# Optimization experiments

Hardware: AMD Instinct MI355X
Metric: run time of the kernel (lower is better)

## Reference

```python
import jax, jax.numpy as jnp
import numpy as np

LATENT, CTX, HID, TDIM, HEADS = 512, 512, 1024, 128, 8
HEAD_DIM = HID // HEADS
SCALE = HEAD_DIM ** -0.5


def _ln(x, g, b, eps=1e-5):
    m = jnp.mean(x, axis=-1, keepdims=True)
    v = jnp.mean((x - m) ** 2, axis=-1, keepdims=True)
    return (x - m) * jax.lax.rsqrt(v + eps) * g + b


def _time_embed(t):
    half = TDIM // 2
    exponent = jnp.linspace(0.0, 1.0, half, dtype=t.dtype)
    freqs = jnp.exp(jnp.log(1000.0) * exponent)
    ang = 2.0 * jnp.pi * t[:, None] * freqs[None, :]
    return jnp.concatenate([jnp.sin(ang), jnp.cos(ang)], axis=-1)  # [B, TDIM]


def setup_inputs() -> dict:
    key = jax.random.key(0)
    ks = iter(jax.random.split(key, 32))
    B, M = 4096, 64

    def w(k, i, o):
        return jax.random.normal(k, (i, o), jnp.float32) * 0.02

    inp = {
        "states": jax.random.normal(next(ks), (B, LATENT), jnp.float32),
        "time_values": jax.random.uniform(next(ks), (B,), jnp.float32),
        "class_summary": jax.random.normal(next(ks), (B, CTX), jnp.float32),
        "support_memory": jax.random.normal(next(ks), (B, M, LATENT), jnp.float32),
        # state_trunk: LN(latent+tdim) -> Linear -> GELU -> Linear
        "trunk_ln_g": jnp.ones((LATENT + TDIM,)), "trunk_ln_b": jnp.zeros((LATENT + TDIM,)),
        "trunk_w1": w(next(ks), LATENT + TDIM, HID), "trunk_b1": jnp.zeros((HID,)),
        "trunk_w2": w(next(ks), HID, HID), "trunk_b2": jnp.zeros((HID,)),
        # memory adapter: LN(latent) -> Linear(latent, hid)
        "mem_ln_g": jnp.ones((LATENT,)), "mem_ln_b": jnp.zeros((LATENT,)),
        "mem_w": w(next(ks), LATENT, HID), "mem_b": jnp.zeros((HID,)),
        # attention projections
        "wq": w(next(ks), HID, HID), "bq": jnp.zeros((HID,)),
        "wk": w(next(ks), HID, HID), "bk": jnp.zeros((HID,)),
        "wv": w(next(ks), HID, HID), "bv": jnp.zeros((HID,)),
        "wo": w(next(ks), HID, HID), "bo": jnp.zeros((HID,)),
        # pre-condition norm + FiLM
        "pre_ln_g": jnp.ones((HID,)), "pre_ln_b": jnp.zeros((HID,)),
        "film_w": w(next(ks), CTX, 2 * HID), "film_b": jnp.zeros((2 * HID,)),
        # conditioner: LN -> Linear -> GELU -> Linear
        "cond_ln_g": jnp.ones((HID,)), "cond_ln_b": jnp.zeros((HID,)),
        "cond_w1": w(next(ks), HID, HID), "cond_b1": jnp.zeros((HID,)),
        "cond_w2": w(next(ks), HID, HID), "cond_b2": jnp.zeros((HID,)),
        # output head: LN -> Linear -> GELU -> Linear(hid, latent)
        "head_ln_g": jnp.ones((HID,)), "head_ln_b": jnp.zeros((HID,)),
        "head_w1": w(next(ks), HID, HID), "head_b1": jnp.zeros((HID,)),
        "head_w2": w(next(ks), HID, LATENT), "head_b2": jnp.zeros((LATENT,)),
    }
    return inp


def _forward(states, time_values, class_summary, support_memory,
             trunk_ln_g, trunk_ln_b, trunk_w1, trunk_b1, trunk_w2, trunk_b2,
             mem_ln_g, mem_ln_b, mem_w, mem_b,
             wq, bq, wk, bk, wv, bv, wo, bo,
             pre_ln_g, pre_ln_b, film_w, film_b,
             cond_ln_g, cond_ln_b, cond_w1, cond_b1, cond_w2, cond_b2,
             head_ln_g, head_ln_b, head_w1, head_b1, head_w2, head_b2):
    B, M, _ = support_memory.shape
    gelu = lambda x: jax.nn.gelu(x, approximate=False)

    # trunk: g = Trunk([y, gamma(t)])
    te = _time_embed(time_values)
    x = _ln(jnp.concatenate([states, te], axis=-1), trunk_ln_g, trunk_ln_b)
    g = gelu(x @ trunk_w1 + trunk_b1) @ trunk_w2 + trunk_b2  # [B, HID]

    # encode memory + single-query multi-head attention
    mem_h = _ln(support_memory, mem_ln_g, mem_ln_b) @ mem_w + mem_b  # [B, M, HID]
    q = (g @ wq + bq).reshape(B, HEADS, HEAD_DIM)
    k = (mem_h @ wk + bk).reshape(B, M, HEADS, HEAD_DIM)
    v = (mem_h @ wv + bv).reshape(B, M, HEADS, HEAD_DIM)
    logits = jnp.einsum("bhd,bmhd->bhm", q, k) * SCALE
    attn = jax.nn.softmax(logits, axis=-1)
    summary = jnp.einsum("bhm,bmhd->bhd", attn, v).reshape(B, HID)
    attn_summary = summary @ wo + bo

    # FiLM conditioning
    combined = _ln(g + attn_summary, pre_ln_g, pre_ln_b)
    film = class_summary @ film_w + film_b
    scale, shift = film[:, :HID], film[:, HID:]
    combined = (1.0 + scale) * combined + shift
    cond_x = _ln(combined, cond_ln_g, cond_ln_b)
    conditioned = gelu(cond_x @ cond_w1 + cond_b1) @ cond_w2 + cond_b2 + combined

    # output head
    hx = _ln(conditioned, head_ln_g, head_ln_b)
    return gelu(hx @ head_w1 + head_b1) @ head_w2 + head_b2  # [B, LATENT]


def reference(states, time_values, class_summary, support_memory,
              trunk_ln_g, trunk_ln_b, trunk_w1, trunk_b1, trunk_w2, trunk_b2,
              mem_ln_g, mem_ln_b, mem_w, mem_b,
              wq, bq, wk, bk, wv, bv, wo, bo,
              pre_ln_g, pre_ln_b, film_w, film_b,
              cond_ln_g, cond_ln_b, cond_w1, cond_b1, cond_w2, cond_b2,
              head_ln_g, head_ln_b, head_w1, head_b1, head_w2, head_b2):
    return _forward(states, time_values, class_summary, support_memory,
                    trunk_ln_g, trunk_ln_b, trunk_w1, trunk_b1, trunk_w2, trunk_b2,
                    mem_ln_g, mem_ln_b, mem_w, mem_b,
                    wq, bq, wk, bk, wv, bv, wo, bo,
                    pre_ln_g, pre_ln_b, film_w, film_b,
                    cond_ln_g, cond_ln_b, cond_w1, cond_b1, cond_w2, cond_b2,
                    head_ln_g, head_ln_b, head_w1, head_b1, head_w2, head_b2)
```

## Files before the change

### kernel.cpp

```cpp
#include <hip/hip_runtime.h>
#include <cstdint>
#include <cstddef>

typedef unsigned short ushort_t;
typedef short s16x8 __attribute__((ext_vector_type(8)));
typedef float f32x4 __attribute__((ext_vector_type(4)));

__device__ __forceinline__ float bf2f(ushort_t h){
  union { unsigned int u; float f; } v; v.u = ((unsigned int)h) << 16; return v.f;
}
__device__ __forceinline__ ushort_t f2bf(float x){
  union { float f; unsigned int u; } v; v.f = x;
  unsigned int r = v.u + 0x7FFFu + ((v.u >> 16) & 1u);
  return (ushort_t)(r >> 16);
}
__device__ __forceinline__ float gelu_f(float x){
  return 0.5f * x * (1.0f + erff(x * 0.7071067811865475f));
}
__device__ __forceinline__ float wave_sum(float v){
  #pragma unroll
  for (int o = 32; o; o >>= 1) v += __shfl_xor(v, o);
  return v;
}
__device__ __forceinline__ void block_reduce2(float& s, float& q, float* red){
  s = wave_sum(s); q = wave_sum(q);
  int w = threadIdx.x >> 6, lane = threadIdx.x & 63, nw = blockDim.x >> 6;
  if (lane == 0){ red[w] = s; red[8 + w] = q; }
  __syncthreads();
  float ts = 0.f, tq = 0.f;
  for (int i = 0; i < nw; ++i){ ts += red[i]; tq += red[8 + i]; }
  __syncthreads();
  s = ts; q = tq;
}

#define SSLOT(cc, m) (((cc) & 56) | (((cc) & 7) ^ (((m) ^ ((m) >> 3)) & 7)))

struct TDesc { const float* in; ushort_t* out; int K; int N; int start; };
struct PrepArgs {
  const float* states; const float* tv; const float* lng; const float* lnb; ushort_t* xnb;
  TDesc t[11];
  int ntiles_end;
  int cast1_blocks;
  int cast_end;
  const float* memw; ushort_t* memwb;
  const float* csum; ushort_t* csb;
  const float* memb; const float* wv; const float* bvp; float* bv2;
};

__global__ __launch_bounds__(256) void prep_k(PrepArgs a){
  int bid = blockIdx.x, tid = threadIdx.x;
  __shared__ float buf[640];
  __shared__ float red[16];
  __shared__ float tbuf[32][33];
  if (bid < 4096){
    int row = bid;
    float t = a.tv[row];
    for (int i = tid; i < 640; i += 256){
      float v;
      if (i < 512) v = a.states[(size_t)row * 512 + i];
      else {
        int j = i - 512, jj = j & 63;
        float fr = expf(6.907755278982137f * ((float)jj * (1.0f / 63.0f)));
        float ang = 6.283185307179586f * t * fr;
        v = (j < 64) ? sinf(ang) : cosf(ang);
      }
      buf[i] = v;
    }
    __syncthreads();
    float s = 0.f, q = 0.f;
    for (int i = tid; i < 640; i += 256){ float v = buf[i]; s += v; q += v * v; }
    block_reduce2(s, q, red);
    float mean = s * (1.0f / 640.0f);
    float var = q * (1.0f / 640.0f) - mean * mean;
    float rstd = rsqrtf(var + 1e-5f);
    for (int i = tid; i < 640; i += 256)
      a.xnb[(size_t)row * 640 + i] = f2bf((buf[i] - mean) * rstd * a.lng[i] + a.lnb[i]);
    return;
  }
  bid -= 4096;
  if (bid < a.ntiles_end){
    int d = 0;
    #pragma unroll
    for (int i = 1; i < 11; ++i) if (bid >= a.t[i].start) d = i;
    TDesc td = a.t[d];
    int tile = bid - td.start;
    int tilesx = td.N >> 5;
    int n0 = (tile % tilesx) << 5, k0 = (tile / tilesx) << 5;
    int tx = tid & 31, ty = tid >> 5;
    #pragma unroll
    for (int j = 0; j < 32; j += 8)
      tbuf[ty + j][tx] = td.in[(size_t)(k0 + ty + j) * td.N + (n0 + tx)];
    __syncthreads();
    #pragma unroll
    for (int j = 0; j < 32; j += 8)
      td.out[(size_t)(n0 + ty + j) * td.K + (k0 + tx)] = f2bf(tbuf[tx][ty + j]);
  } else if (bid < a.cast_end){
    int ci = bid - a.ntiles_end;
    const float* src; ushort_t* dst; int i;
    if (ci < a.cast1_blocks){ src = a.memw; dst = a.memwb; i = ci * 1024 + tid * 4; }
    else { src = a.csum; dst = a.csb; i = (ci - a.cast1_blocks) * 1024 + tid * 4; }
    float4 v = *(const float4*)(src + i);
    union { ushort_t u[4]; uint2 p; } pk;
    pk.u[0] = f2bf(v.x); pk.u[1] = f2bf(v.y); pk.u[2] = f2bf(v.z); pk.u[3] = f2bf(v.w);
    *(uint2*)(dst + i) = pk.p;
  } else {
    int col = (bid - a.cast_end) * 256 + tid;
    float a0 = 0.f, a1 = 0.f, a2 = 0.f, a3 = 0.f;
    for (int j = 0; j < 1024; j += 4){
      a0 += a.memb[j + 0] * a.wv[(size_t)(j + 0) * 1024 + col];
      a1 += a.memb[j + 1] * a.wv[(size_t)(j + 1) * 1024 + col];
      a2 += a.memb[j + 2] * a.wv[(size_t)(j + 2) * 1024 + col];
      a3 += a.memb[j + 3] * a.wv[(size_t)(j + 3) * 1024 + col];
    }
    a.bv2[col] = a0 + a1 + a2 + a3 + a.bvp[col];
  }
}

__global__ __launch_bounds__(256) void ln_rows_k(const ushort_t* __restrict__ in, const float* __restrict__ g,
    const float* __restrict__ b, ushort_t* __restrict__ out, int D){
  int row = blockIdx.x, tid = threadIdx.x, i = tid * 4;
  __shared__ float red[16];
  union { uint2 p; ushort_t u[4]; } vv;
  vv.p = *(const uint2*)(in + (size_t)row * D + i);
  float v[4] = { bf2f(vv.u[0]), bf2f(vv.u[1]), bf2f(vv.u[2]), bf2f(vv.u[3]) };
  float s = v[0] + v[1] + v[2] + v[3];
  float q = v[0]*v[0] + v[1]*v[1] + v[2]*v[2] + v[3]*v[3];
  block_reduce2(s, q, red);
  float invD = 1.0f / (float)D;
  float mean = s * invD, var = q * invD - mean * mean, rstd = rsqrtf(var + 1e-5f);
  union { ushort_t u[4]; uint2 p; } pk;
  #pragma unroll
  for (int e = 0; e < 4; ++e) pk.u[e] = f2bf((v[e] - mean) * rstd * g[i + e] + b[i + e]);
  *(uint2*)(out + (size_t)row * D + i) = pk.p;
}

__global__ __launch_bounds__(256) void fuse_film_k(const ushort_t* __restrict__ combb, const ushort_t* __restrict__ filmb,
    const float* __restrict__ pg, const float* __restrict__ pb,
    const float* __restrict__ cg, const float* __restrict__ cb,
    ushort_t* __restrict__ c2b, ushort_t* __restrict__ cxb){
  int row = blockIdx.x, tid = threadIdx.x, i = tid * 4;
  __shared__ float red[16];
  union { uint2 p; ushort_t u[4]; } av;
  av.p = *(const uint2*)(combb + (size_t)row * 1024 + i);
  float x[4] = { bf2f(av.u[0]), bf2f(av.u[1]), bf2f(av.u[2]), bf2f(av.u[3]) };
  float s = x[0] + x[1] + x[2] + x[3];
  float q = x[0]*x[0] + x[1]*x[1] + x[2]*x[2] + x[3]*x[3];
  block_reduce2(s, q, red);
  float mean = s * (1.0f / 1024.0f), var = q * (1.0f / 1024.0f) - mean * mean;
  float rstd = rsqrtf(var + 1e-5f);
  float4 pgv = *(const float4*)(pg + i), pbv = *(const float4*)(pb + i);
  union { uint2 p; ushort_t u[4]; } scv, shv;
  scv.p = *(const uint2*)(filmb + (size_t)row * 2048 + i);
  shv.p = *(const uint2*)(filmb + (size_t)row * 2048 + 1024 + i);
  float c2[4];
  {
    float pgx[4] = { pgv.x, pgv.y, pgv.z, pgv.w };
    float pbx[4] = { pbv.x, pbv.y, pbv.z, pbv.w };
    #pragma unroll
    for (int e = 0; e < 4; ++e){
      float cc = (x[e] - mean) * rstd * pgx[e] + pbx[e];
      c2[e] = (1.0f + bf2f(scv.u[e])) * cc + bf2f(shv.u[e]);
    }
  }
  union { ushort_t u[4]; uint2 p; } pc;
  #pragma unroll
  for (int e = 0; e < 4; ++e) pc.u[e] = f2bf(c2[e]);
  *(uint2*)(c2b + (size_t)row * 1024 + i) = pc.p;
  float s2 = c2[0] + c2[1] + c2[2] + c2[3];
  float q2 = c2[0]*c2[0] + c2[1]*c2[1] + c2[2]*c2[2] + c2[3]*c2[3];
  block_reduce2(s2, q2, red);
  float m2 = s2 * (1.0f / 1024.0f), v2 = q2 * (1.0f / 1024.0f) - m2 * m2;
  float r2 = rsqrtf(v2 + 1e-5f);
  float4 cgv = *(const float4*)(cg + i), cbv = *(const float4*)(cb + i);
  union { ushort_t u[4]; uint2 p; } pk;
  pk.u[0] = f2bf((c2[0] - m2) * r2 * cgv.x + cbv.x);
  pk.u[1] = f2bf((c2[1] - m2) * r2 * cgv.y + cbv.y);
  pk.u[2] = f2bf((c2[2] - m2) * r2 * cgv.z + cbv.z);
  pk.u[3] = f2bf((c2[3] - m2) * r2 * cgv.w + cbv.w);
  *(uint2*)(cxb + (size_t)row * 1024 + i) = pk.p;
}

__global__ __launch_bounds__(256, 2) void suppattn_k(
    const float* __restrict__ support, const float* __restrict__ lgw, const float* __restrict__ lbw,
    const ushort_t* __restrict__ U, ushort_t* __restrict__ R)
{
  __shared__ ushort_t S[64 * 512];
  __shared__ ushort_t UG[9 * 512];
  __shared__ float WTf[8][65];
  __shared__ float SUMV[64], SUMSQ[64];
  __shared__ __align__(16) float MEANR[64];
  __shared__ __align__(16) float RSTDR[64];
  __shared__ float PMAX[4][8], PSUM[4][8], PMU[4][8];
  __shared__ float AB[2][8];
  __shared__ float MUH[8];

  int bb = blockIdx.x, tid = threadIdx.x, w = tid >> 6, l = tid & 63;
  const ushort_t* Ub = U + (size_t)bb * 4096;

  for (int id = tid; id < 576; id += 256){
    int hr8 = id >> 6, cc = id & 63;
    int byteoff = hr8 * 1024 + (((cc & 56) | ((cc & 7) ^ (hr8 & 7))) << 4);
    uint4* dst = (uint4*)((char*)UG + byteoff);
    if (hr8 < 8){
      s16x8 uv = *(const s16x8*)(Ub + hr8 * 512 + cc * 8);
      float4 g0 = *(const float4*)(lgw + cc * 8);
      float4 g1 = *(const float4*)(lgw + cc * 8 + 4);
      float ga[8] = { g0.x, g0.y, g0.z, g0.w, g1.x, g1.y, g1.z, g1.w };
      union { ushort_t u[8]; uint4 p; } pk;
      #pragma unroll
      for (int e = 0; e < 8; ++e) pk.u[e] = f2bf(ga[e] * bf2f((ushort_t)uv[e]));
      *dst = pk.p;
    } else {
      *dst = make_uint4(0x3F803F80u, 0x3F803F80u, 0x3F803F80u, 0x3F803F80u);
    }
  }

  {
    int h0 = 2 * w, h1 = 2 * w + 1;
    s16x8 u0 = *(const s16x8*)(Ub + h0 * 512 + l * 8);
    s16x8 u1 = *(const s16x8*)(Ub + h1 * 512 + l * 8);
    float4 g0 = *(const float4*)(lgw + l * 8), g1 = *(const float4*)(lgw + l * 8 + 4);
    float4 c0 = *(const float4*)(lbw + l * 8), c1 = *(const float4*)(lbw + l * 8 + 4);
    float ga[8] = { g0.x, g0.y, g0.z, g0.w, g1.x, g1.y, g1.z, g1.w };
    float ba[8] = { c0.x, c0.y, c0.z, c0.w, c1.x, c1.y, c1.z, c1.w };
    float A0 = 0.f, B0 = 0.f, A1 = 0.f, B1 = 0.f;
    #pragma unroll
    for (int e = 0; e < 8; ++e){
      float x0 = bf2f((ushort_t)u0[e]), x1 = bf2f((ushort_t)u1[e]);
      A0 += ba[e] * x0; B0 += ga[e] * x0;
      A1 += ba[e] * x1; B1 += ga[e] * x1;
    }
    A0 = wave_sum(A0); B0 = wave_sum(B0); A1 = wave_sum(A1); B1 = wave_sum(B1);
    if (l == 0){ AB[0][h0] = A0; AB[1][h0] = B0; AB[0][h1] = A1; AB[1][h1] = B1; }
  }

  #pragma unroll 4
  for (int i = 0; i < 16; ++i){
    int m = i * 4 + w;
    const float* row = support + ((size_t)bb * 64 + m) * 512 + l * 8;
    float4 a0 = *(const float4*)row, a1 = *(const float4*)(row + 4);
    union { ushort_t u[8]; uint4 p; } pk;
    pk.u[0] = f2bf(a0.x); pk.u[1] = f2bf(a0.y); pk.u[2] = f2bf(a0.z); pk.u[3] = f2bf(a0.w);
    pk.u[4] = f2bf(a1.x); pk.u[5] = f2bf(a1.y); pk.u[6] = f2bf(a1.z); pk.u[7] = f2bf(a1.w);
    int byteoff = m * 1024 + (SSLOT(l, m) << 4);
    *(uint4*)((char*)S + byteoff) = pk.p;
  }
  __syncthreads();

  int l15 = l & 15, lk = l >> 4;
  int hr = (l15 < 8) ? l15 : 8;
  int arowb = (w * 16 + l15) * 1024;
  int hrowb = hr * 1024;
  int am = w * 16 + l15;
  f32x4 dacc = (f32x4){0.f, 0.f, 0.f, 0.f};
  f32x4 sacc = (f32x4){0.f, 0.f, 0.f, 0.f};
  #pragma unroll
  for (int ks = 0; ks < 16; ++ks){
    int cc = ks * 4 + lk;
    s16x8 afr = *(const s16x8*)((char*)S + arowb + (SSLOT(cc, am) << 4));
    s16x8 bfr = *(const s16x8*)((char*)UG + hrowb + (((cc & 56) | ((cc & 7) ^ (hr & 7))) << 4));
    dacc = __builtin_amdgcn_mfma_f32_16x16x32_bf16(afr, bfr, dacc, 0, 0, 0);
    sacc = __builtin_amdgcn_mfma_f32_16x16x32_bf16(afr, afr, sacc, 0, 0, 0);
  }
  if (l15 == 8){
    #pragma unroll
    for (int j = 0; j < 4; ++j) SUMV[w * 16 + lk * 4 + j] = dacc[j];
  }
  if ((l15 >> 2) == lk) SUMSQ[w * 16 + l15] = sacc[l15 & 3];
  __syncthreads();
  if (tid < 64){
    float mean = SUMV[tid] * (1.0f / 512.0f);
    float var = SUMSQ[tid] * (1.0f / 512.0f) - mean * mean;
    MEANR[tid] = mean;
    RSTDR[tid] = rsqrtf(var + 1e-5f);
  }
  __syncthreads();

  int r0 = w * 16 + lk * 4;
  float4 mns = *(const float4*)(MEANR + r0);
  float4 rst = *(const float4*)(RSTDR + r0);
  float mn[4] = { mns.x, mns.y, mns.z, mns.w };
  float rs[4] = { rst.x, rst.y, rst.z, rst.w };
  float Ah = AB[0][l15 & 7], Bh = AB[1][l15 & 7];
  float lg[4];
  #pragma unroll
  for (int j = 0; j < 4; ++j)
    lg[j] = 0.08838834764831845f * (rs[j] * (dacc[j] - mn[j] * Bh) + Ah);
  float lmax = fmaxf(fmaxf(lg[0], lg[1]), fmaxf(lg[2], lg[3]));
  lmax = fmaxf(lmax, __shfl_xor(lmax, 16));
  lmax = fmaxf(lmax, __shfl_xor(lmax, 32));
  if (l < 8) PMAX[w][l] = lmax;
  __syncthreads();
  float gmax = fmaxf(fmaxf(PMAX[0][l15 & 7], PMAX[1][l15 & 7]),
                     fmaxf(PMAX[2][l15 & 7], PMAX[3][l15 & 7]));
  float e4[4]; float ls = 0.f, lm = 0.f;
  #pragma unroll
  for (int j = 0; j < 4; ++j){
    e4[j] = __expf(lg[j] - gmax);
    ls += e4[j];
    lm += e4[j] * rs[j] * mn[j];
  }
  ls += __shfl_xor(ls, 16); ls += __shfl_xor(ls, 32);
  lm += __shfl_xor(lm, 16); lm += __shfl_xor(lm, 32);
  if (l < 8){ PSUM[w][l] = ls; PMU[w][l] = lm; }
  __syncthreads();
  float Sh = PSUM[0][l15 & 7] + PSUM[1][l15 & 7] + PSUM[2][l15 & 7] + PSUM[3][l15 & 7];
  float inv = 1.0f / Sh;
  if (l15 < 8){
    #pragma unroll
    for (int j = 0; j < 4; ++j) WTf[l15][r0 + j] = e4[j] * rs[j] * inv;
  }
  if (w == 0 && l < 8){
    MUH[l] = (PMU[0][l] + PMU[1][l] + PMU[2][l] + PMU[3][l]) * inv;
  }
  __syncthreads();

  union { ushort_t u[8]; s16x8 v; } af0, af1;
  af0.v = (s16x8){0,0,0,0,0,0,0,0};
  af1.v = (s16x8){0,0,0,0,0,0,0,0};
  if (l15 < 8){
    #pragma unroll
    for (int e = 0; e < 8; ++e){
      af0.u[e] = f2bf(WTf[l15][lk * 8 + e]);
      af1.u[e] = f2bf(WTf[l15][32 + lk * 8 + e]);
    }
  }
  float mu[4];
  #pragma unroll
  for (int j = 0; j < 4; ++j) mu[j] = (lk < 2) ? MUH[lk * 4 + j] : 0.f;

  const char* Sp = (const char*)S;
  #pragma unroll
  for (int ns = 0; ns < 8; ++ns){
    int c = w * 128 + ns * 16 + l15;
    int cch = c >> 3, cb = (c & 7) * 2;
    int sb = cch & 56, cl = cch & 7;
    union { ushort_t u[8]; s16x8 v; } bf0, bf1;
    #pragma unroll
    for (int e = 0; e < 8; ++e){
      int m0 = lk * 8 + e;
      int m1 = m0 + 32;
      bf0.u[e] = *(const ushort_t*)(Sp + m0 * 1024 + ((sb | (cl ^ ((m0 ^ lk) & 7))) << 4) + cb);
      bf1.u[e] = *(const ushort_t*)(Sp + m1 * 1024 + ((sb | (cl ^ ((m1 ^ (4 + lk)) & 7))) << 4) + cb);
    }
    f32x4 cacc = (f32x4){0.f, 0.f, 0.f, 0.f};
    cacc = __builtin_amdgcn_mfma_f32_16x16x32_bf16(af0.v, bf0.v, cacc, 0, 0, 0);
    cacc = __builtin_amdgcn_mfma_f32_16x16x32_bf16(af1.v, bf1.v, cacc, 0, 0, 0);
    if (lk < 2){
      float gc = lgw[c], bc = lbw[c];
      #pragma unroll
      for (int j = 0; j < 4; ++j){
        int h = lk * 4 + j;
        R[(size_t)bb * 4096 + h * 512 + c] = f2bf(gc * (cacc[j] - mu[j]) + bc);
      }
    }
  }
}

#define GLL16(gsrc, ldst) \
  __builtin_amdgcn_global_load_lds((const __attribute__((address_space(1))) unsigned int*)(gsrc), \
                                   (__attribute__((address_space(3))) unsigned int*)(ldst), 16, 0, 0)

template<bool GELU, bool BIAS, bool WF32, bool WBF16, bool RESID>
__global__ __launch_bounds__(256, 3) void gemm_k(
    const ushort_t* __restrict__ A, int lda, long long aZ,
    const ushort_t* __restrict__ Bt, int ldb, long long bZ,
    const float* __restrict__ bias, long long biasZ,
    float* __restrict__ C, int ldc, long long cZ,
    ushort_t* __restrict__ Cb, int ldcb, long long cbZ,
    const ushort_t* __restrict__ R, int ldr,
    int M, int N, int K)
{
  __shared__ ushort_t smA[2][64 * 64];
  __shared__ ushort_t smB[2][128 * 64];
  int tid = threadIdx.x, lane = tid & 63, w = tid >> 6;
  int z = blockIdx.z;
  A  += (size_t)aZ * z;
  Bt += (size_t)bZ * z;
  if (BIAS)  bias += (size_t)biasZ * z;
  if (WF32)  C    += (size_t)cZ * z;
  if (WBF16) Cb   += (size_t)cbZ * z;

  int gx = gridDim.x, gy = gridDim.y;
  int nwg = gx * gy;
  int bx = blockIdx.x, by = blockIdx.y;
  if ((nwg & 7) == 0 && (gx & (gx - 1)) == 0){
    int lid = bx + gx * by;
    int cpx = nwg >> 3;
    int slid = (lid & 7) * cpx + (lid >> 3);
    int lgx = 31 - __clz(gx);
    bx = slid & (gx - 1);
    by = slid >> lgx;
  }
  int m0 = by * 64, n0 = bx * 128;
  int nk = K >> 6;

  auto stage = [&](int buf, int kt){
    int k0 = kt << 6;
    #pragma unroll
    for (int i = 0; i < 2; ++i){
      int c = ((w << 1) + i) * 64 + lane;
      int rowl = c >> 3, sp = c & 7;
      int sg = sp ^ (rowl & 7);
      GLL16(A + (size_t)(m0 + rowl) * lda + (k0 + sg * 8), &smA[buf][((w << 1) + i) * 512]);
    }
    #pragma unroll
    for (int i = 0; i < 4; ++i){
      int c = ((w << 2) + i) * 64 + lane;
      int rowl = c >> 3, sp = c & 7;
      int sg = sp ^ (rowl & 7);
      GLL16(Bt + (size_t)(n0 + rowl) * ldb + (k0 + sg * 8), &smB[buf][((w << 2) + i) * 512]);
    }
  };

  int qrow = w >> 1, qcol = w & 1;
  int l15 = lane & 15, lk = lane >> 4, l7 = lane & 7;
  int sb0 = ((0 + lk) ^ l7) << 4;
  int sb1 = ((4 + lk) ^ l7) << 4;
  int arow = (qrow * 32 + l15) * 128;
  int brow = (qcol * 64 + l15) * 128;

  f32x4 acc[2][4];
  #pragma unroll
  for (int m = 0; m < 2; ++m)
    #pragma unroll
    for (int n = 0; n < 4; ++n)
      acc[m][n] = (f32x4){0.f, 0.f, 0.f, 0.f};

  stage(0, 0);
  asm volatile("s_waitcnt vmcnt(0)" ::: "memory");
  __syncthreads();
  for (int kt = 0; kt < nk; ++kt){
    int cur = kt & 1;
    if (kt + 1 < nk) stage((kt + 1) & 1, kt + 1);
    const char* ab = (const char*)&smA[cur][0];
    const char* bbp = (const char*)&smB[cur][0];
    s16x8 af[2][2], bfv[4][2];
    #pragma unroll
    for (int m = 0; m < 2; ++m){
      af[m][0] = *(const s16x8*)(ab + arow + m * 2048 + sb0);
      af[m][1] = *(const s16x8*)(ab + arow + m * 2048 + sb1);
    }
    #pragma unroll
    for (int n = 0; n < 4; ++n){
      bfv[n][0] = *(const s16x8*)(bbp + brow + n * 2048 + sb0);
      bfv[n][1] = *(const s16x8*)(bbp + brow + n * 2048 + sb1);
    }
    #pragma unroll
    for (int kb = 0; kb < 2; ++kb)
      #pragma unroll
      for (int m = 0; m < 2; ++m)
        #pragma unroll
        for (int n = 0; n < 4; ++n)
          acc[m][n] = __builtin_amdgcn_mfma_f32_16x16x32_bf16(af[m][kb], bfv[n][kb], acc[m][n], 0, 0, 0);
    asm volatile("s_waitcnt vmcnt(0)" ::: "memory");
    __syncthreads();
  }

  #pragma unroll
  for (int n = 0; n < 4; ++n){
    int col = n0 + qcol * 64 + n * 16 + l15;
    float bvv = BIAS ? bias[col] : 0.0f;
    #pragma unroll
    for (int m = 0; m < 2; ++m){
      int rbase = m0 + qrow * 32 + m * 16 + lk * 4;
      #pragma unroll
      for (int r = 0; r < 4; ++r){
        float x = acc[m][n][r] + bvv;
        if (GELU) x = gelu_f(x);
        int row = rbase + r;
        if (RESID) x += bf2f(R[(size_t)row * ldr + col]);
        if (WF32)  C[(size_t)row * ldc + col] = x;
        if (WBF16) Cb[(size_t)row * ldcb + col] = f2bf(x);
      }
    }
  }
}

extern "C" void kernel_launch(void* const* d_in, const int* in_sizes, int n_in,
                              void* d_out, int out_size, void* d_ws, size_t ws_size,
                              hipStream_t stream)
{
  (void)in_sizes; (void)n_in; (void)out_size;
  const float* states      = (const float*)d_in[0];
  const float* time_values = (const float*)d_in[1];
  const float* class_sum   = (const float*)d_in[2];
  const float* support     = (const float*)d_in[3];
  const float* trunk_ln_g  = (const float*)d_in[4];
  const float* trunk_ln_b  = (const float*)d_in[5];
  const float* trunk_w1    = (const float*)d_in[6];
  const float* trunk_b1    = (const float*)d_in[7];
  const float* trunk_w2    = (const float*)d_in[8];
  const float* trunk_b2    = (const float*)d_in[9];
  const float* mem_ln_g    = (const float*)d_in[10];
  const float* mem_ln_b    = (const float*)d_in[11];
  const float* mem_w       = (const float*)d_in[12];
  const float* mem_b       = (const float*)d_in[13];
  const float* wq          = (const float*)d_in[14];
  const float* bq          = (const float*)d_in[15];
  const float* wk          = (const float*)d_in[16];
  const float* wv          = (const float*)d_in[18];
  const float* bvp         = (const float*)d_in[19];
  const float* wo          = (const float*)d_in[20];
  const float* bo          = (const float*)d_in[21];
  const float* pre_g       = (const float*)d_in[22];
  const float* pre_b       = (const float*)d_in[23];
  const float* film_w      = (const float*)d_in[24];
  const float* film_b      = (const float*)d_in[25];
  const float* cond_g      = (const float*)d_in[26];
  const float* cond_b      = (const float*)d_in[27];
  const float* cond_w1     = (const float*)d_in[28];
  const float* cond_b1     = (const float*)d_in[29];
  const float* cond_w2     = (const float*)d_in[30];
  const float* cond_b2     = (const float*)d_in[31];
  const float* head_g      = (const float*)d_in[32];
  const float* head_bb     = (const float*)d_in[33];
  const float* head_w1     = (const float*)d_in[34];
  const float* head_b1     = (const float*)d_in[35];
  const float* head_w2     = (const float*)d_in[36];
  const float* head_b2     = (const float*)d_in[37];
  float* out = (float*)d_out;

  char* ws = (char*)d_ws;
  size_t off = 0;
  auto alloc = [&](size_t bytes)->char*{
    char* p = ws + off;
    off += (bytes + 255) & ~(size_t)255;
    return p;
  };
  ushort_t* tw1T   = (ushort_t*)alloc((size_t)640 * 1024 * 2);
  ushort_t* tw2T   = (ushort_t*)alloc((size_t)1024 * 1024 * 2);
  ushort_t* wqT    = (ushort_t*)alloc((size_t)1024 * 1024 * 2);
  ushort_t* wkT    = (ushort_t*)alloc((size_t)1024 * 1024 * 2);
  ushort_t* wvT    = (ushort_t*)alloc((size_t)1024 * 1024 * 2);
  ushort_t* woT    = (ushort_t*)alloc((size_t)1024 * 1024 * 2);
  ushort_t* memw_b = (ushort_t*)alloc((size_t)512 * 1024 * 2);
  ushort_t* filmWT = (ushort_t*)alloc((size_t)512 * 2048 * 2);
  ushort_t* cw1T   = (ushort_t*)alloc((size_t)1024 * 1024 * 2);
  ushort_t* cw2T   = (ushort_t*)alloc((size_t)1024 * 1024 * 2);
  ushort_t* hw1T   = (ushort_t*)alloc((size_t)1024 * 1024 * 2);
  ushort_t* hw2T   = (ushort_t*)alloc((size_t)1024 * 512 * 2);
  ushort_t* K2     = (ushort_t*)alloc((size_t)512 * 1024 * 2);
  ushort_t* V2T    = (ushort_t*)alloc((size_t)1024 * 512 * 2);
  float*    bv2    = (float*)   alloc((size_t)1024 * 4);
  ushort_t* xnb    = (ushort_t*)alloc((size_t)4096 * 640 * 2);
  ushort_t* h1     = (ushort_t*)alloc((size_t)4096 * 1024 * 2);
  ushort_t* gb     = (ushort_t*)alloc((size_t)4096 * 1024 * 2);
  ushort_t* qb     = (ushort_t*)alloc((size_t)4096 * 1024 * 2);
  ushort_t* U      = (ushort_t*)alloc((size_t)4096 * 4096 * 2);
  ushort_t* Rb     = (ushort_t*)alloc((size_t)4096 * 4096 * 2);
  ushort_t* sumb   = (ushort_t*)alloc((size_t)4096 * 1024 * 2);
  ushort_t* combb  = (ushort_t*)alloc((size_t)4096 * 1024 * 2);
  ushort_t* csb    = (ushort_t*)alloc((size_t)4096 * 512 * 2);
  ushort_t* filmb  = (ushort_t*)alloc((size_t)4096 * 2048 * 2);
  ushort_t* c2b    = (ushort_t*)alloc((size_t)4096 * 1024 * 2);
  ushort_t* cxb    = (ushort_t*)alloc((size_t)4096 * 1024 * 2);
  ushort_t* c1     = (ushort_t*)alloc((size_t)4096 * 1024 * 2);
  ushort_t* cond2b = (ushort_t*)alloc((size_t)4096 * 1024 * 2);
  ushort_t* hxb    = (ushort_t*)alloc((size_t)4096 * 1024 * 2);
  ushort_t* h3     = (ushort_t*)alloc((size_t)4096 * 1024 * 2);
  if (off > ws_size) return;

  PrepArgs pa;
  pa.states = states; pa.tv = time_values; pa.lng = trunk_ln_g; pa.lnb = trunk_ln_b; pa.xnb = xnb;
  int s = 0;
  auto setT = [&](int i, const float* in, ushort_t* o, int K, int N){
    pa.t[i].in = in; pa.t[i].out = o; pa.t[i].K = K; pa.t[i].N = N; pa.t[i].start = s;
    s += (N >> 5) * (K >> 5);
  };
  setT(0, trunk_w1, tw1T, 640, 1024);
  setT(1, trunk_w2, tw2T, 1024, 1024);
  setT(2, wq, wqT, 1024, 1024);
  setT(3, wk, wkT, 1024, 1024);
  setT(4, wv, wvT, 1024, 1024);
  setT(5, wo, woT, 1024, 1024);
  setT(6, film_w, filmWT, 512, 2048);
  setT(7, cond_w1, cw1T, 1024, 1024);
  setT(8, cond_w2, cw2T, 1024, 1024);
  setT(9, head_w1, hw1T, 1024, 1024);
  setT(10, head_w2, hw2T, 1024, 512);
  pa.ntiles_end = s;
  pa.cast1_blocks = (512 * 1024) / 1024;
  pa.cast_end = s + pa.cast1_blocks + (4096 * 512) / 1024;
  pa.memw = mem_w; pa.memwb = memw_b;
  pa.csum = class_sum; pa.csb = csb;
  pa.memb = mem_b; pa.wv = wv; pa.bvp = bvp; pa.bv2 = bv2;
  prep_k<<<4096 + pa.cast_end + 4, 256, 0, stream>>>(pa);

  gemm_k<false, false, false, true, false><<<dim3(8, 8, 1), 256, 0, stream>>>(
      memw_b, 1024, 0, wkT, 1024, 0, nullptr, 0, nullptr, 0, 0, K2, 1024, 0, nullptr, 0, 512, 1024, 1024);
  gemm_k<false, false, false, true, false><<<dim3(4, 16, 1), 256, 0, stream>>>(
      wvT, 1024, 0, memw_b, 1024, 0, nullptr, 0, nullptr, 0, 0, V2T, 512, 0, nullptr, 0, 1024, 512, 1024);

  gemm_k<true, true, false, true, false><<<dim3(8, 64, 1), 256, 0, stream>>>(
      xnb, 640, 0, tw1T, 640, 0, trunk_b1, 0, nullptr, 0, 0, h1, 1024, 0, nullptr, 0, 4096, 1024, 640);
  gemm_k<false, true, false, true, false><<<dim3(8, 64, 1), 256, 0, stream>>>(
      h1, 1024, 0, tw2T, 1024, 0, trunk_b2, 0, nullptr, 0, 0, gb, 1024, 0, nullptr, 0, 4096, 1024, 1024);
  gemm_k<false, true, false, true, false><<<dim3(8, 64, 1), 256, 0, stream>>>(
      gb, 1024, 0, wqT, 1024, 0, bq, 0, nullptr, 0, 0, qb, 1024, 0, nullptr, 0, 4096, 1024, 1024);
  gemm_k<false, false, false, true, false><<<dim3(4, 64, 8), 256, 0, stream>>>(
      qb, 1024, 128, K2, 1024, 128, nullptr, 0, nullptr, 0, 0, U, 4096, 512, nullptr, 0, 4096, 512, 128);

  suppattn_k<<<4096, 256, 0, stream>>>(support, mem_ln_g, mem_ln_b, U, Rb);

  gemm_k<false, true, false, true, false><<<dim3(1, 64, 8), 256, 0, stream>>>(
      Rb, 4096, 512, V2T, 512, 65536, bv2, 128, nullptr, 0, 0, sumb, 1024, 128, nullptr, 0, 4096, 128, 512);

  gemm_k<false, true, false, true, true><<<dim3(8, 64, 1), 256, 0, stream>>>(
      sumb, 1024, 0, woT, 1024, 0, bo, 0, nullptr, 0, 0, combb, 1024, 0, gb, 1024, 4096, 1024, 1024);
  gemm_k<false, true, false, true, false><<<dim3(16, 64, 1), 256, 0, stream>>>(
      csb, 512, 0, filmWT, 512, 0, film_b, 0, nullptr, 0, 0, filmb, 2048, 0, nullptr, 0, 4096, 2048, 512);

  fuse_film_k<<<4096, 256, 0, stream>>>(combb, filmb, pre_g, pre_b, cond_g, cond_b, c2b, cxb);

  gemm_k<true, true, false, true, false><<<dim3(8, 64, 1), 256, 0, stream>>>(
      cxb, 1024, 0, cw1T, 1024, 0, cond_b1, 0, nullptr, 0, 0, c1, 1024, 0, nullptr, 0, 4096, 1024, 1024);
  gemm_k<false, true, false, true, true><<<dim3(8, 64, 1), 256, 0, stream>>>(
      c1, 1024, 0, cw2T, 1024, 0, cond_b2, 0, nullptr, 0, 0, cond2b, 1024, 0, c2b, 1024, 4096, 1024, 1024);
  ln_rows_k<<<4096, 256, 0, stream>>>(cond2b, head_g, head_bb, hxb, 1024);
  gemm_k<true, true, false, true, false><<<dim3(8, 64, 1), 256, 0, stream>>>(
      hxb, 1024, 0, hw1T, 1024, 0, head_b1, 0, nullptr, 0, 0, h3, 1024, 0, nullptr, 0, 4096, 1024, 1024);
  gemm_k<false, true, true, false, false><<<dim3(4, 64, 1), 256, 0, stream>>>(
      h3, 1024, 0, hw2T, 1024, 0, head_b2, 0, out, 512, 0, nullptr, 0, 0, nullptr, 0, 4096, 512, 1024);
}
```

Before: 451.8 us.

## Shrink GEMM tiles to 64x64 with triple-buffered pipeline and grouped GEMM launches

Changes the GEMM tile from 64x128 to 64x64 and moves from a double-buffered to a triple-buffered shared-memory pipeline that waits on partial vmcnt, so loads for the next tile overlap the current compute. Independent GEMMs (K/V weight projections with trunk layer 1, and Q projection with FiLM) are merged into a single grouped launch using per-segment descriptors. In the support-attention kernel the support-row load is moved ahead of the U staging so its global latency is exposed earlier. Smaller tiles double the block count and lower per-block B reuse, in exchange for better occupancy and fewer launches.

Result: slower. 469.1 us (+3.8%).

```diff
diff --git a/kernel.cpp b/kernel.cpp
--- a/kernel.cpp
+++ b/kernel.cpp
@@ -197,6 +197,18 @@
   int bb = blockIdx.x, tid = threadIdx.x, w = tid >> 6, l = tid & 63;
   const ushort_t* Ub = U + (size_t)bb * 4096;
 
+  #pragma unroll 4
+  for (int i = 0; i < 16; ++i){
+    int m = i * 4 + w;
+    const float* row = support + ((size_t)bb * 64 + m) * 512 + l * 8;
+    float4 a0 = *(const float4*)row, a1 = *(const float4*)(row + 4);
+    union { ushort_t u[8]; uint4 p; } pk;
+    pk.u[0] = f2bf(a0.x); pk.u[1] = f2bf(a0.y); pk.u[2] = f2bf(a0.z); pk.u[3] = f2bf(a0.w);
+    pk.u[4] = f2bf(a1.x); pk.u[5] = f2bf(a1.y); pk.u[6] = f2bf(a1.z); pk.u[7] = f2bf(a1.w);
+    int byteoff = m * 1024 + (SSLOT(l, m) << 4);
+    *(uint4*)((char*)S + byteoff) = pk.p;
+  }
+
   for (int id = tid; id < 576; id += 256){
     int hr8 = id >> 6, cc = id & 63;
     int byteoff = hr8 * 1024 + (((cc & 56) | ((cc & 7) ^ (hr8 & 7))) << 4);
@@ -233,18 +245,6 @@
     A0 = wave_sum(A0); B0 = wave_sum(B0); A1 = wave_sum(A1); B1 = wave_sum(B1);
     if (l == 0){ AB[0][h0] = A0; AB[1][h0] = B0; AB[0][h1] = A1; AB[1][h1] = B1; }
   }
-
-  #pragma unroll 4
-  for (int i = 0; i < 16; ++i){
-    int m = i * 4 + w;
-    const float* row = support + ((size_t)bb * 64 + m) * 512 + l * 8;
-    float4 a0 = *(const float4*)row, a1 = *(const float4*)(row + 4);
-    union { ushort_t u[8]; uint4 p; } pk;
-    pk.u[0] = f2bf(a0.x); pk.u[1] = f2bf(a0.y); pk.u[2] = f2bf(a0.z); pk.u[3] = f2bf(a0.w);
-    pk.u[4] = f2bf(a1.x); pk.u[5] = f2bf(a1.y); pk.u[6] = f2bf(a1.z); pk.u[7] = f2bf(a1.w);
-    int byteoff = m * 1024 + (SSLOT(l, m) << 4);
-    *(uint4*)((char*)S + byteoff) = pk.p;
-  }
   __syncthreads();
 
   int l15 = l & 15, lk = l >> 4;
@@ -361,6 +361,124 @@
   __builtin_amdgcn_global_load_lds((const __attribute__((address_space(1))) unsigned int*)(gsrc), \
                                    (__attribute__((address_space(3))) unsigned int*)(ldst), 16, 0, 0)
 
+struct GDesc {
+  const ushort_t* A; const ushort_t* Bt; const float* bias;
+  ushort_t* Cb; const ushort_t* R;
+  int lda, ldb, ldcb, ldr;
+  int gx, startBlock, flags, K;
+};
+struct GSet { GDesc d[3]; int nseg; };
+
+#define GEMM64_BODY(APTR, BPTR, LDA, LDB, KVAL)                                             \
+  int nk = (KVAL) >> 6;                                                                     \
+  auto stage = [&](int buf, int kt){                                                        \
+    int k0 = kt << 6;                                                                       \
+    _Pragma("unroll")                                                                       \
+    for (int i = 0; i < 2; ++i){                                                            \
+      int c = ((w << 1) + i) * 64 + lane;                                                   \
+      int rowl = c >> 3, sp = c & 7;                                                        \
+      int sg = sp ^ (rowl & 7);                                                             \
+      GLL16((APTR) + (size_t)(m0 + rowl) * (LDA) + (k0 + sg * 8), &smA[buf][((w << 1) + i) * 512]); \
+    }                                                                                       \
+    _Pragma("unroll")                                                                       \
+    for (int i = 0; i < 2; ++i){                                                            \
+      int c = ((w << 1) + i) * 64 + lane;                                                   \
+      int rowl = c >> 3, sp = c & 7;                                                        \
+      int sg = sp ^ (rowl & 7);                                                             \
+      GLL16((BPTR) + (size_t)(n0 + rowl) * (LDB) + (k0 + sg * 8), &smB[buf][((w << 1) + i) * 512]); \
+    }                                                                                       \
+  };                                                                                        \
+  int qrow = w >> 1, qcol = w & 1;                                                          \
+  int l15 = lane & 15, lk = lane >> 4, l7 = lane & 7;                                       \
+  int sb0 = ((0 + lk) ^ l7) << 4;                                                           \
+  int sb1 = ((4 + lk) ^ l7) << 4;                                                           \
+  int arow = (qrow * 32 + l15) * 128;                                                       \
+  int brow = (qcol * 32 + l15) * 128;                                                       \
+  f32x4 acc[2][2];                                                                          \
+  _Pragma("unroll")                                                                         \
+  for (int m = 0; m < 2; ++m)                                                               \
+    _Pragma("unroll")                                                                       \
+    for (int n = 0; n < 2; ++n)                                                             \
+      acc[m][n] = (f32x4){0.f, 0.f, 0.f, 0.f};                                              \
+  stage(0, 0);                                                                              \
+  if (nk > 1){                                                                              \
+    stage(1, 1);                                                                            \
+    asm volatile("s_waitcnt vmcnt(4)" ::: "memory");       \
+  } else {                                                                                  \
+    asm volatile("s_waitcnt vmcnt(0)" ::: "memory");                                        \
+  }                                                                                         \
+  __syncthreads();                                                                          \
+  int cur = 0, st = 2;                                                                      \
+  for (int kt = 0; kt < nk; ++kt){                                                          \
+    if (kt + 2 < nk) stage(st, kt + 2);                                                     \
+    const char* ab = (const char*)&smA[cur][0];                                             \
+    const char* bbp = (const char*)&smB[cur][0];                                            \
+    s16x8 af[2][2], bfv[2][2];                                                              \
+    _Pragma("unroll")                                                                       \
+    for (int m = 0; m < 2; ++m){                                                            \
+      af[m][0] = *(const s16x8*)(ab + arow + m * 2048 + sb0);                               \
+      af[m][1] = *(const s16x8*)(ab + arow + m * 2048 + sb1);                               \
+    }                                                                                       \
+    _Pragma("unroll")                                                                       \
+    for (int n = 0; n < 2; ++n){                                                            \
+      bfv[n][0] = *(const s16x8*)(bbp + brow + n * 2048 + sb0);                             \
+      bfv[n][1] = *(const s16x8*)(bbp + brow + n * 2048 + sb1);                             \
+    }                                                                                       \
+    _Pragma("unroll")                                                                       \
+    for (int kb = 0; kb < 2; ++kb)                                                          \
+      _Pragma("unroll")                                                                     \
+      for (int m = 0; m < 2; ++m)                                                           \
+        _Pragma("unroll")                                                                   \
+        for (int n = 0; n < 2; ++n)                                                         \
+          acc[m][n] = __builtin_amdgcn_mfma_f32_16x16x32_bf16(af[m][kb], bfv[n][kb], acc[m][n], 0, 0, 0); \
+    if (kt + 1 < nk){                                                                       \
+      if (kt + 2 < nk) asm volatile("s_waitcnt vmcnt(4)" ::: "memory");                     \
+      else             asm volatile("s_waitcnt vmcnt(0)" ::: "memory");                     \
+      __syncthreads();                                                                      \
+    }                                                                                       \
+    cur = (cur == 2) ? 0 : cur + 1;                                                         \
+    st  = (st  == 2) ? 0 : st  + 1;                                                         \
+  }
+
+__global__ __launch_bounds__(256, 3) void gemmset_k(GSet gs){
+  __shared__ ushort_t smA[3][64 * 64];
+  __shared__ ushort_t smB[3][64 * 64];
+  int bid = blockIdx.x, tid = threadIdx.x, lane = tid & 63, w = tid >> 6;
+  int seg = 0;
+  #pragma unroll
+  for (int i = 1; i < 3; ++i) if (i < gs.nseg && bid >= gs.d[i].startBlock) seg = i;
+  GDesc g = gs.d[seg];
+  int lid = bid - g.startBlock;
+  {
+    int nwg = (seg + 1 < gs.nseg ? gs.d[seg + 1].startBlock : (int)gridDim.x) - g.startBlock;
+    int q = nwg >> 3;
+    lid = (lid & 7) * q + (lid >> 3);
+  }
+  int bx = lid % g.gx, by = lid / g.gx;
+  int m0 = by * 64, n0 = bx * 64;
+
+  GEMM64_BODY(g.A, g.Bt, g.lda, g.ldb, g.K)
+
+  bool fGELU = g.flags & 1, fBIAS = g.flags & 2, fRES = g.flags & 16;
+  #pragma unroll
+  for (int n = 0; n < 2; ++n){
+    int col = n0 + qcol * 32 + n * 16 + l15;
+    float bvv = fBIAS ? g.bias[col] : 0.0f;
+    #pragma unroll
+    for (int m = 0; m < 2; ++m){
+      int rbase = m0 + qrow * 32 + m * 16 + lk * 4;
+      #pragma unroll
+      for (int r = 0; r < 4; ++r){
+        float x = acc[m][n][r] + bvv;
+        if (fGELU) x = gelu_f(x);
+        int row = rbase + r;
+        if (fRES) x += bf2f(g.R[(size_t)row * g.ldr + col]);
+        g.Cb[(size_t)row * g.ldcb + col] = f2bf(x);
+      }
+    }
+  }
+}
+
 template<bool GELU, bool BIAS, bool WF32, bool WBF16, bool RESID>
 __global__ __launch_bounds__(256, 3) void gemm_k(
     const ushort_t* __restrict__ A, int lda, long long aZ,
@@ -371,8 +489,8 @@
     const ushort_t* __restrict__ R, int ldr,
     int M, int N, int K)
 {
-  __shared__ ushort_t smA[2][64 * 64];
-  __shared__ ushort_t smB[2][128 * 64];
+  __shared__ ushort_t smA[3][64 * 64];
+  __shared__ ushort_t smB[3][64 * 64];
   int tid = threadIdx.x, lane = tid & 63, w = tid >> 6;
   int z = blockIdx.z;
   A  += (size_t)aZ * z;
@@ -392,74 +510,13 @@
     bx = slid & (gx - 1);
     by = slid >> lgx;
   }
-  int m0 = by * 64, n0 = bx * 128;
-  int nk = K >> 6;
-
-  auto stage = [&](int buf, int kt){
-    int k0 = kt << 6;
-    #pragma unroll
-    for (int i = 0; i < 2; ++i){
-      int c = ((w << 1) + i) * 64 + lane;
-      int rowl = c >> 3, sp = c & 7;
-      int sg = sp ^ (rowl & 7);
-      GLL16(A + (size_t)(m0 + rowl) * lda + (k0 + sg * 8), &smA[buf][((w << 1) + i) * 512]);
-    }
-    #pragma unroll
-    for (int i = 0; i < 4; ++i){
-      int c = ((w << 2) + i) * 64 + lane;
-      int rowl = c >> 3, sp = c & 7;
-      int sg = sp ^ (rowl & 7);
-      GLL16(Bt + (size_t)(n0 + rowl) * ldb + (k0 + sg * 8), &smB[buf][((w << 2) + i) * 512]);
-    }
-  };
-
-  int qrow = w >> 1, qcol = w & 1;
-  int l15 = lane & 15, lk = lane >> 4, l7 = lane & 7;
-  int sb0 = ((0 + lk) ^ l7) << 4;
-  int sb1 = ((4 + lk) ^ l7) << 4;
-  int arow = (qrow * 32 + l15) * 128;
-  int brow = (qcol * 64 + l15) * 128;
-
-  f32x4 acc[2][4];
-  #pragma unroll
-  for (int m = 0; m < 2; ++m)
-    #pragma unroll
-    for (int n = 0; n < 4; ++n)
-      acc[m][n] = (f32x4){0.f, 0.f, 0.f, 0.f};
-
-  stage(0, 0);
-  asm volatile("s_waitcnt vmcnt(0)" ::: "memory");
-  __syncthreads();
-  for (int kt = 0; kt < nk; ++kt){
-    int cur = kt & 1;
-    if (kt + 1 < nk) stage((kt + 1) & 1, kt + 1);
-    const char* ab = (const char*)&smA[cur][0];
-    const char* bbp = (const char*)&smB[cur][0];
-    s16x8 af[2][2], bfv[4][2];
-    #pragma unroll
-    for (int m = 0; m < 2; ++m){
-      af[m][0] = *(const s16x8*)(ab + arow + m * 2048 + sb0);
-      af[m][1] = *(const s16x8*)(ab + arow + m * 2048 + sb1);
-    }
-    #pragma unroll
-    for (int n = 0; n < 4; ++n){
-      bfv[n][0] = *(const s16x8*)(bbp + brow + n * 2048 + sb0);
-      bfv[n][1] = *(const s16x8*)(bbp + brow + n * 2048 + sb1);
-    }
-    #pragma unroll
-    for (int kb = 0; kb < 2; ++kb)
-      #pragma unroll
-      for (int m = 0; m < 2; ++m)
-        #pragma unroll
-        for (int n = 0; n < 4; ++n)
-          acc[m][n] = __builtin_amdgcn_mfma_f32_16x16x32_bf16(af[m][kb], bfv[n][kb], acc[m][n], 0, 0, 0);
-    asm volatile("s_waitcnt vmcnt(0)" ::: "memory");
-    __syncthreads();
-  }
-
-  #pragma unroll
-  for (int n = 0; n < 4; ++n){
-    int col = n0 + qcol * 64 + n * 16 + l15;
+  int m0 = by * 64, n0 = bx * 64;
+
+  GEMM64_BODY(A, Bt, lda, ldb, K)
+
+  #pragma unroll
+  for (int n = 0; n < 2; ++n){
+    int col = n0 + qcol * 32 + n * 16 + l15;
     float bvv = BIAS ? bias[col] : 0.0f;
     #pragma unroll
     for (int m = 0; m < 2; ++m){
@@ -587,39 +644,45 @@
   pa.memb = mem_b; pa.wv = wv; pa.bvp = bvp; pa.bv2 = bv2;
   prep_k<<<4096 + pa.cast_end + 4, 256, 0, stream>>>(pa);
 
-  gemm_k<false, false, false, true, false><<<dim3(8, 8, 1), 256, 0, stream>>>(
-      memw_b, 1024, 0, wkT, 1024, 0, nullptr, 0, nullptr, 0, 0, K2, 1024, 0, nullptr, 0, 512, 1024, 1024);
-  gemm_k<false, false, false, true, false><<<dim3(4, 16, 1), 256, 0, stream>>>(
-      wvT, 1024, 0, memw_b, 1024, 0, nullptr, 0, nullptr, 0, 0, V2T, 512, 0, nullptr, 0, 1024, 512, 1024);
-
-  gemm_k<true, true, false, true, false><<<dim3(8, 64, 1), 256, 0, stream>>>(
-      xnb, 640, 0, tw1T, 640, 0, trunk_b1, 0, nullptr, 0, 0, h1, 1024, 0, nullptr, 0, 4096, 1024, 640);
-  gemm_k<false, true, false, true, false><<<dim3(8, 64, 1), 256, 0, stream>>>(
+  {
+    GSet gs; gs.nseg = 3;
+    gs.d[0] = { memw_b, wkT, nullptr, K2, nullptr, 1024, 1024, 1024, 0, 16, 0, 8, 1024 };
+    gs.d[1] = { wvT, memw_b, nullptr, V2T, nullptr, 1024, 1024, 512, 0, 8, 128, 8, 1024 };
+    gs.d[2] = { xnb, tw1T, trunk_b1, h1, nullptr, 640, 640, 1024, 0, 16, 256, 1|2|8, 640 };
+    gemmset_k<<<1280, 256, 0, stream>>>(gs);
+  }
+
+  gemm_k<false, true, false, true, false><<<dim3(16, 64, 1), 256, 0, stream>>>(
       h1, 1024, 0, tw2T, 1024, 0, trunk_b2, 0, nullptr, 0, 0, gb, 1024, 0, nullptr, 0, 4096, 1024, 1024);
-  gemm_k<false, true, false, true, false><<<dim3(8, 64, 1), 256, 0, stream>>>(
-      gb, 1024, 0, wqT, 1024, 0, bq, 0, nullptr, 0, 0, qb, 1024, 0, nullptr, 0, 4096, 1024, 1024);
-  gemm_k<false, false, false, true, false><<<dim3(4, 64, 8), 256, 0, stream>>>(
+
+  {
+    GSet gs; gs.nseg = 2;
+    gs.d[0] = { gb, wqT, bq, qb, nullptr, 1024, 1024, 1024, 0, 16, 0, 2|8, 1024 };
+    gs.d[1] = { csb, filmWT, film_b, filmb, nullptr, 512, 512, 2048, 0, 32, 1024, 2|8, 512 };
+    gs.d[2] = gs.d[1];
+    gemmset_k<<<3072, 256, 0, stream>>>(gs);
+  }
+
+  gemm_k<false, false, false, true, false><<<dim3(8, 64, 8), 256, 0, stream>>>(
       qb, 1024, 128, K2, 1024, 128, nullptr, 0, nullptr, 0, 0, U, 4096, 512, nullptr, 0, 4096, 512, 128);
 
   suppattn_k<<<4096, 256, 0, stream>>>(support, mem_ln_g, mem_ln_b, U, Rb);
 
-  gemm_k<false, true, false, true, false><<<dim3(1, 64, 8), 256, 0, stream>>>(
+  gemm_k<false, true, false, true, false><<<dim3(2, 64, 8), 256, 0, stream>>>(
       Rb, 4096, 512, V2T, 512, 65536, bv2, 128, nullptr, 0, 0, sumb, 1024, 128, nullptr, 0, 4096, 128, 512);
 
-  gemm_k<false, true, false, true, true><<<dim3(8, 64, 1), 256, 0, stream>>>(
+  gemm_k<false, true, false, true, true><<<dim3(16, 64, 1), 256, 0, stream>>>(
       sumb, 1024, 0, woT, 1024, 0, bo, 0, nullptr, 0, 0, combb, 1024, 0, gb, 1024, 4096, 1024, 1024);
-  gemm_k<false, true, false, true, false><<<dim3(16, 64, 1), 256, 0, stream>>>(
-      csb, 512, 0, filmWT, 512, 0, film_b, 0, nullptr, 0, 0, filmb, 2048, 0, nullptr, 0, 4096, 2048, 512);
 
   fuse_film_k<<<4096, 256, 0, stream>>>(combb, filmb, pre_g, pre_b, cond_g, cond_b, c2b, cxb);
 
-  gemm_k<true, true, false, true, false><<<dim3(8, 64, 1), 256, 0, stream>>>(
+  gemm_k<true, true, false, true, false><<<dim3(16, 64, 1), 256, 0, stream>>>(
       cxb, 1024, 0, cw1T, 1024, 0, cond_b1, 0, nullptr, 0, 0, c1, 1024, 0, nullptr, 0, 4096, 1024, 1024);
-  gemm_k<false, true, false, true, true><<<dim3(8, 64, 1), 256, 0, stream>>>(
+  gemm_k<false, true, false, true, true><<<dim3(16, 64, 1), 256, 0, stream>>>(
       c1, 1024, 0, cw2T, 1024, 0, cond_b2, 0, nullptr, 0, 0, cond2b, 1024, 0, c2b, 1024, 4096, 1024, 1024);
   ln_rows_k<<<4096, 256, 0, stream>>>(cond2b, head_g, head_bb, hxb, 1024);
-  gemm_k<true, true, false, true, false><<<dim3(8, 64, 1), 256, 0, stream>>>(
+  gemm_k<true, true, false, true, false><<<dim3(16, 64, 1), 256, 0, stream>>>(
       hxb, 1024, 0, hw1T, 1024, 0, head_b1, 0, nullptr, 0, 0, h3, 1024, 0, nullptr, 0, 4096, 1024, 1024);
-  gemm_k<false, true, true, false, false><<<dim3(4, 64, 1), 256, 0, stream>>>(
+  gemm_k<false, true, true, false, false><<<dim3(8, 64, 1), 256, 0, stream>>>(
       h3, 1024, 0, hw2T, 1024, 0, head_b2, 0, out, 512, 0, nullptr, 0, 0, nullptr, 0, 4096, 512, 1024);
 }
```
